# Optimization experiments

Measured on AMD Instinct MI355X. Metric: run time of the kernel, lower is better.

The kernel has to match this reference:

```python
import jax, jax.numpy as jnp
import numpy as np

# ---- static hash-grid config (mirrors init_kwargs) ----
RANGE = 1.0
DIM = 3
N_LEVELS = 16
F_PER_LEVEL = 2
LOG2_HASHMAP = 15
HASHMAP_SIZE = 1 << LOG2_HASHMAP
BASE_RES = 16
FINEST_RES = 512
RANK = 4
PRIMES = np.array([1, 2654435761, 805459861], dtype=np.uint32)


def _resolutions():
    # N_l = floor(base * b^l), b = exp((ln(Nmax)-ln(Nmin))/(L-1))  (Instant-NGP eq. 2-3)
    b = np.exp((np.log(FINEST_RES) - np.log(BASE_RES)) / (N_LEVELS - 1))
    return np.floor(BASE_RES * b ** np.arange(N_LEVELS)).astype(np.float32)


def setup_inputs() -> dict:
    key = jax.random.key(0)
    k1, k2, k3 = jax.random.split(key, 3)
    x = jax.random.uniform(k1, (524288, DIM), dtype=jnp.float32)  # in [-range, range]
    # LoRA factors; small init like hash-grid tables (~1e-2 scale)
    table_A = jax.random.normal(k2, (N_LEVELS, HASHMAP_SIZE, RANK), dtype=jnp.float32) * 1e-2
    table_B = jax.random.normal(k3, (N_LEVELS, RANK, F_PER_LEVEL), dtype=jnp.float32) * 1e-1
    return {"x": x, "table_A": table_A, "table_B": table_B}


def reference(x, table_A, table_B):
    # wrapper: normalize to [0,1]
    xn = (x + RANGE) / (2.0 * RANGE)                         # [N,3]
    res = jnp.asarray(_resolutions())                        # [L]

    # materialize tiny per-level tables from LoRA factors: [L, S, F]
    tables = jnp.einsum('lsr,lrf->lsf', table_A, table_B)

    xl = xn[None, :, :] * res[:, None, None]                 # [L,N,3]
    xf = jnp.floor(xl)
    w = xl - xf                                              # [L,N,3] trilinear weights
    xi = xf.astype(jnp.uint32)                               # [L,N,3]

    # 2^3 corner offsets
    corners = jnp.array([[(c >> d) & 1 for d in range(DIM)] for c in range(2 ** DIM)],
                        dtype=jnp.uint32)                    # [8,3]

    pos = xi[:, :, None, :] + corners[None, None, :, :]      # [L,N,8,3]
    primes = jnp.asarray(PRIMES)
    h = (pos[..., 0] * primes[0]) ^ (pos[..., 1] * primes[1]) ^ (pos[..., 2] * primes[2])
    idx = (h & jnp.uint32(HASHMAP_SIZE - 1)).astype(jnp.int32)  # [L,N,8]

    # per-level gather: [L,N,8,F]
    feats = jax.vmap(lambda t, i: t[i])(tables, idx)

    # trilinear weights per corner: prod over dims of (w or 1-w)
    wc = jnp.prod(jnp.where(corners[None, None, :, :] == 1,
                            w[:, :, None, :], 1.0 - w[:, :, None, :]), axis=-1)  # [L,N,8]

    out_l = jnp.sum(feats * wc[..., None], axis=2)           # [L,N,F]
    out = jnp.transpose(out_l, (1, 0, 2)).reshape(x.shape[0], N_LEVELS * F_PER_LEVEL)
    return out.astype(jnp.float32)
```

## Files before the change

kernel.cpp:

```cpp
#include <hip/hip_runtime.h>
#include <hip/hip_fp16.h>
#include <math.h>
#include <stdint.h>
#include <stddef.h>

#define NLEVELS 16
#define HSIZE   32768
#define LOGH    15
#define RANKK   4
#define PRIME1  2654435761u
#define PRIME2  805459861u

#define BLK2 1024
#define PPB  8192

struct ResArr { float v[NLEVELS]; };

__global__ void build_tables_k(const float* __restrict__ A, const float* __restrict__ B,
                               uint32_t* __restrict__ T) {
    int i = blockIdx.x * blockDim.x + threadIdx.x;
    if (i >= NLEVELS * HSIZE) return;
    int l = i >> LOGH;
    const float4 a = *reinterpret_cast<const float4*>(A + (size_t)i * RANKK);
    const float* b = B + l * (RANKK * 2);
    float f0 = a.x * b[0] + a.y * b[2] + a.z * b[4] + a.w * b[6];
    float f1 = a.x * b[1] + a.y * b[3] + a.z * b[5] + a.w * b[7];
    __half2 h = __floats2half2_rn(f0, f1);
    T[i] = *reinterpret_cast<uint32_t*>(&h);
}

__global__ __launch_bounds__(BLK2)
void encode_level_k(const float* __restrict__ x, const uint32_t* __restrict__ T,
                    float* __restrict__ dst_base, int nPoints, int directOut,
                    ResArr res) {
    __shared__ uint32_t lds[HSIZE];
    const int l     = blockIdx.x & (NLEVELS - 1);
    const int chunk = blockIdx.x >> 4;

    const uint32_t* Tl = T + (size_t)l * HSIZE;
    for (int i = threadIdx.x; i < HSIZE / 4; i += BLK2) {
        reinterpret_cast<uint4*>(lds)[i] = reinterpret_cast<const uint4*>(Tl)[i];
    }
    __syncthreads();

    const float r = res.v[l];
    const int base = chunk * PPB;
    float* dst;
    size_t stride;
    if (directOut) { dst = dst_base + 2 * l;                      stride = 32; }
    else           { dst = dst_base + (size_t)l * nPoints * 2;    stride = 2;  }

    for (int k = 0; k < PPB; k += BLK2) {
        int n = base + k + (int)threadIdx.x;
        if (n >= nPoints) break;
        float xn0 = (x[3 * n + 0] + 1.0f) * 0.5f;
        float xn1 = (x[3 * n + 1] + 1.0f) * 0.5f;
        float xn2 = (x[3 * n + 2] + 1.0f) * 0.5f;
        float xl0 = xn0 * r, xl1 = xn1 * r, xl2 = xn2 * r;
        float fl0 = floorf(xl0), fl1 = floorf(xl1), fl2 = floorf(xl2);
        float w0 = xl0 - fl0, w1 = xl1 - fl1, w2 = xl2 - fl2;
        uint32_t i0 = (uint32_t)fl0, i1 = (uint32_t)fl1, i2 = (uint32_t)fl2;

        uint32_t hx0 = i0,          hx1 = i0 + 1u;
        uint32_t hy0 = i1 * PRIME1, hy1 = hy0 + PRIME1;
        uint32_t hz0 = i2 * PRIME2, hz1 = hz0 + PRIME2;

        float w0a = 1.0f - w0, w1a = 1.0f - w1, w2a = 1.0f - w2;
        float wxy00 = w0a * w1a, wxy10 = w0 * w1a, wxy01 = w0a * w1, wxy11 = w0 * w1;

        float acc0 = 0.0f, acc1 = 0.0f;
#pragma unroll
        for (int c = 0; c < 8; ++c) {
            uint32_t h = ((c & 1) ? hx1 : hx0) ^ ((c & 2) ? hy1 : hy0) ^ ((c & 4) ? hz1 : hz0);
            uint32_t pk = lds[h & (HSIZE - 1)];
            __half2 h2 = *reinterpret_cast<__half2*>(&pk);
            float2 f = __half22float2(h2);
            float wxy = (c & 2) ? ((c & 1) ? wxy11 : wxy01) : ((c & 1) ? wxy10 : wxy00);
            float wc = wxy * ((c & 4) ? w2 : w2a);
            acc0 = fmaf(f.x, wc, acc0);
            acc1 = fmaf(f.y, wc, acc1);
        }
        *reinterpret_cast<float2*>(dst + (size_t)n * stride) = make_float2(acc0, acc1);
    }
}

__global__ void merge_k(const float* __restrict__ outT, float* __restrict__ out, int nPoints) {
    int n = blockIdx.x * blockDim.x + threadIdx.x;
    if (n >= nPoints) return;
    const float2* src = reinterpret_cast<const float2*>(outT);
    float4 o[8];
#pragma unroll
    for (int q = 0; q < 8; ++q) {
        float2 a = src[(size_t)(2 * q)     * nPoints + n];
        float2 b = src[(size_t)(2 * q + 1) * nPoints + n];
        o[q] = make_float4(a.x, a.y, b.x, b.y);
    }
    float4* dstv = reinterpret_cast<float4*>(out + (size_t)n * 32);
#pragma unroll
    for (int q = 0; q < 8; ++q) dstv[q] = o[q];
}

__global__ void encode_fallback_k(const float* __restrict__ x, const float* __restrict__ A,
                                  const float* __restrict__ B, float* __restrict__ out,
                                  int nPoints, ResArr res) {
    int n = blockIdx.x * blockDim.x + threadIdx.x;
    if (n >= nPoints) return;
    float xn0 = (x[3 * n + 0] + 1.0f) * 0.5f;
    float xn1 = (x[3 * n + 1] + 1.0f) * 0.5f;
    float xn2 = (x[3 * n + 2] + 1.0f) * 0.5f;
    for (int l = 0; l < NLEVELS; ++l) {
        float r = res.v[l];
        float xl0 = xn0 * r, xl1 = xn1 * r, xl2 = xn2 * r;
        float fl0 = floorf(xl0), fl1 = floorf(xl1), fl2 = floorf(xl2);
        float w0 = xl0 - fl0, w1 = xl1 - fl1, w2 = xl2 - fl2;
        uint32_t i0 = (uint32_t)fl0, i1 = (uint32_t)fl1, i2 = (uint32_t)fl2;
        uint32_t hx0 = i0,          hx1 = i0 + 1u;
        uint32_t hy0 = i1 * PRIME1, hy1 = hy0 + PRIME1;
        uint32_t hz0 = i2 * PRIME2, hz1 = hz0 + PRIME2;
        float w0a = 1.0f - w0, w1a = 1.0f - w1, w2a = 1.0f - w2;
        float wxy00 = w0a * w1a, wxy10 = w0 * w1a, wxy01 = w0a * w1, wxy11 = w0 * w1;
        const float* b = B + l * 8;
        float b00 = b[0], b01 = b[1], b10 = b[2], b11 = b[3];
        float b20 = b[4], b21 = b[5], b30 = b[6], b31 = b[7];
        float acc0 = 0.0f, acc1 = 0.0f;
#pragma unroll
        for (int c = 0; c < 8; ++c) {
            uint32_t h = ((c & 1) ? hx1 : hx0) ^ ((c & 2) ? hy1 : hy0) ^ ((c & 4) ? hz1 : hz0);
            uint32_t idx = h & (HSIZE - 1);
            float4 a = *reinterpret_cast<const float4*>(A + ((size_t)l * HSIZE + idx) * RANKK);
            float fe0 = a.x * b00 + a.y * b10 + a.z * b20 + a.w * b30;
            float fe1 = a.x * b01 + a.y * b11 + a.z * b21 + a.w * b31;
            float wxy = (c & 2) ? ((c & 1) ? wxy11 : wxy01) : ((c & 1) ? wxy10 : wxy00);
            float wc = wxy * ((c & 4) ? w2 : w2a);
            acc0 = fmaf(fe0, wc, acc0);
            acc1 = fmaf(fe1, wc, acc1);
        }
        out[(size_t)n * 32 + 2 * l + 0] = acc0;
        out[(size_t)n * 32 + 2 * l + 1] = acc1;
    }
}

extern "C" void kernel_launch(void* const* d_in, const int* in_sizes, int n_in,
                              void* d_out, int out_size, void* d_ws, size_t ws_size,
                              hipStream_t stream) {
    const float* x = (const float*)d_in[0];
    const float* A = (const float*)d_in[1];
    const float* B = (const float*)d_in[2];
    float* out = (float*)d_out;
    int nPoints = in_sizes[0] / 3;

    ResArr ra;
    {
        double b = exp((log(512.0) - log(16.0)) / 15.0);
        for (int l = 0; l < NLEVELS; ++l)
            ra.v[l] = (float)floor(16.0 * pow(b, (double)l));
    }

    const size_t tblBytes  = (size_t)NLEVELS * HSIZE * sizeof(uint32_t);
    const size_t outTBytes = (size_t)NLEVELS * (size_t)nPoints * 2 * sizeof(float);

    if (ws_size >= tblBytes) {
        uint32_t* T = (uint32_t*)d_ws;
        int nb1 = (NLEVELS * HSIZE + 255) / 256;
        build_tables_k<<<nb1, 256, 0, stream>>>(A, B, T);
        int chunks = (nPoints + PPB - 1) / PPB;
        if (ws_size >= tblBytes + outTBytes) {
            float* outT = (float*)((char*)d_ws + tblBytes);
            encode_level_k<<<chunks * NLEVELS, BLK2, 0, stream>>>(x, T, outT, nPoints, 0, ra);
            merge_k<<<(nPoints + 255) / 256, 256, 0, stream>>>(outT, out, nPoints);
        } else {
            encode_level_k<<<chunks * NLEVELS, BLK2, 0, stream>>>(x, T, out, nPoints, 1, ra);
        }
    } else {
        encode_fallback_k<<<(nPoints + 255) / 256, 256, 0, stream>>>(x, A, B, out, nPoints, ra);
    }
}
```

Before: 138.6 us.

## Fuse all levels into one kernel per point block with async LDS loads

Replaces the per-level encode kernel and the separate transpose/merge kernel with a single kernel. Each block keeps its points in registers and iterates over all 16 levels, streaming each level's half-precision table into LDS via global_load_lds. Each block then writes the full 32-float output row directly. This removes the intermediate level-major buffer and its extra write/read pass. In exchange, every block reloads all 16 tables, and table loads are serialized with compute behind barriers, with only one block per CU.

```diff
diff --git a/kernel.cpp b/kernel.cpp
--- a/kernel.cpp
+++ b/kernel.cpp
@@ -11,10 +11,14 @@
 #define PRIME1  2654435761u
 #define PRIME2  805459861u
 
-#define BLK2 1024
-#define PPB  8192
+#define BLK  1024
+#define PTS  2
+#define PPB  (BLK * PTS)
 
 struct ResArr { float v[NLEVELS]; };
+
+typedef __attribute__((address_space(1))) const uint32_t gu32;
+typedef __attribute__((address_space(3))) uint32_t lu32;
 
 __global__ void build_tables_k(const float* __restrict__ A, const float* __restrict__ B,
                                uint32_t* __restrict__ T) {
@@ -29,75 +33,86 @@
     T[i] = *reinterpret_cast<uint32_t*>(&h);
 }
 
-__global__ __launch_bounds__(BLK2)
-void encode_level_k(const float* __restrict__ x, const uint32_t* __restrict__ T,
-                    float* __restrict__ dst_base, int nPoints, int directOut,
-                    ResArr res) {
+__global__ __launch_bounds__(BLK)
+void encode_all_k(const float* __restrict__ x, const uint32_t* __restrict__ T,
+                  float* __restrict__ out, int nPoints, ResArr res) {
     __shared__ uint32_t lds[HSIZE];
-    const int l     = blockIdx.x & (NLEVELS - 1);
-    const int chunk = blockIdx.x >> 4;
+    const int t    = threadIdx.x;
+    const int base = blockIdx.x * PPB;
 
-    const uint32_t* Tl = T + (size_t)l * HSIZE;
-    for (int i = threadIdx.x; i < HSIZE / 4; i += BLK2) {
-        reinterpret_cast<uint4*>(lds)[i] = reinterpret_cast<const uint4*>(Tl)[i];
+    int   n[PTS];
+    bool  valid[PTS];
+    float xn0[PTS], xn1[PTS], xn2[PTS];
+#pragma unroll
+    for (int p = 0; p < PTS; ++p) {
+        n[p] = base + p * BLK + t;
+        valid[p] = (n[p] < nPoints);
+        int m = valid[p] ? n[p] : 0;
+        xn0[p] = (x[3 * m + 0] + 1.0f) * 0.5f;
+        xn1[p] = (x[3 * m + 1] + 1.0f) * 0.5f;
+        xn2[p] = (x[3 * m + 2] + 1.0f) * 0.5f;
     }
-    __syncthreads();
 
-    const float r = res.v[l];
-    const int base = chunk * PPB;
-    float* dst;
-    size_t stride;
-    if (directOut) { dst = dst_base + 2 * l;                      stride = 32; }
-    else           { dst = dst_base + (size_t)l * nPoints * 2;    stride = 2;  }
+    float acc[PTS][NLEVELS * 2];
+#pragma unroll
+    for (int p = 0; p < PTS; ++p)
+#pragma unroll
+        for (int q = 0; q < NLEVELS * 2; ++q) acc[p][q] = 0.0f;
 
-    for (int k = 0; k < PPB; k += BLK2) {
-        int n = base + k + (int)threadIdx.x;
-        if (n >= nPoints) break;
-        float xn0 = (x[3 * n + 0] + 1.0f) * 0.5f;
-        float xn1 = (x[3 * n + 1] + 1.0f) * 0.5f;
-        float xn2 = (x[3 * n + 2] + 1.0f) * 0.5f;
-        float xl0 = xn0 * r, xl1 = xn1 * r, xl2 = xn2 * r;
-        float fl0 = floorf(xl0), fl1 = floorf(xl1), fl2 = floorf(xl2);
-        float w0 = xl0 - fl0, w1 = xl1 - fl1, w2 = xl2 - fl2;
-        uint32_t i0 = (uint32_t)fl0, i1 = (uint32_t)fl1, i2 = (uint32_t)fl2;
+#pragma unroll
+    for (int l = 0; l < NLEVELS; ++l) {
+        if (l) __syncthreads();
+        {
+            const uint32_t* Tl = T + (size_t)l * HSIZE;
+#pragma unroll
+            for (int k = 0; k < HSIZE / (BLK * 4); ++k) {
+                int i = (k * BLK + t) * 4;
+                __builtin_amdgcn_global_load_lds((gu32*)(Tl + i), (lu32*)(lds + i), 16, 0, 0);
+            }
+        }
+        __syncthreads();
 
-        uint32_t hx0 = i0,          hx1 = i0 + 1u;
-        uint32_t hy0 = i1 * PRIME1, hy1 = hy0 + PRIME1;
-        uint32_t hz0 = i2 * PRIME2, hz1 = hz0 + PRIME2;
+        const float r = res.v[l];
+#pragma unroll
+        for (int p = 0; p < PTS; ++p) {
+            float xl0 = xn0[p] * r, xl1 = xn1[p] * r, xl2 = xn2[p] * r;
+            float fl0 = floorf(xl0), fl1 = floorf(xl1), fl2 = floorf(xl2);
+            float w0 = xl0 - fl0, w1 = xl1 - fl1, w2 = xl2 - fl2;
+            uint32_t i0 = (uint32_t)fl0, i1 = (uint32_t)fl1, i2 = (uint32_t)fl2;
 
-        float w0a = 1.0f - w0, w1a = 1.0f - w1, w2a = 1.0f - w2;
-        float wxy00 = w0a * w1a, wxy10 = w0 * w1a, wxy01 = w0a * w1, wxy11 = w0 * w1;
+            uint32_t hx0 = i0,          hx1 = i0 + 1u;
+            uint32_t hy0 = i1 * PRIME1, hy1 = hy0 + PRIME1;
+            uint32_t hz0 = i2 * PRIME2, hz1 = hz0 + PRIME2;
 
-        float acc0 = 0.0f, acc1 = 0.0f;
+            float w0a = 1.0f - w0, w1a = 1.0f - w1, w2a = 1.0f - w2;
+            float wxy00 = w0a * w1a, wxy10 = w0 * w1a, wxy01 = w0a * w1, wxy11 = w0 * w1;
+
+            float a0 = 0.0f, a1 = 0.0f;
 #pragma unroll
-        for (int c = 0; c < 8; ++c) {
-            uint32_t h = ((c & 1) ? hx1 : hx0) ^ ((c & 2) ? hy1 : hy0) ^ ((c & 4) ? hz1 : hz0);
-            uint32_t pk = lds[h & (HSIZE - 1)];
-            __half2 h2 = *reinterpret_cast<__half2*>(&pk);
-            float2 f = __half22float2(h2);
-            float wxy = (c & 2) ? ((c & 1) ? wxy11 : wxy01) : ((c & 1) ? wxy10 : wxy00);
-            float wc = wxy * ((c & 4) ? w2 : w2a);
-            acc0 = fmaf(f.x, wc, acc0);
-            acc1 = fmaf(f.y, wc, acc1);
+            for (int c = 0; c < 8; ++c) {
+                uint32_t h = ((c & 1) ? hx1 : hx0) ^ ((c & 2) ? hy1 : hy0) ^ ((c & 4) ? hz1 : hz0);
+                uint32_t pk = lds[h & (HSIZE - 1)];
+                __half2 h2 = *reinterpret_cast<__half2*>(&pk);
+                float2 f = __half22float2(h2);
+                float wxy = (c & 2) ? ((c & 1) ? wxy11 : wxy01) : ((c & 1) ? wxy10 : wxy00);
+                float wc = wxy * ((c & 4) ? w2 : w2a);
+                a0 = fmaf(f.x, wc, a0);
+                a1 = fmaf(f.y, wc, a1);
+            }
+            acc[p][2 * l + 0] = a0;
+            acc[p][2 * l + 1] = a1;
         }
-        *reinterpret_cast<float2*>(dst + (size_t)n * stride) = make_float2(acc0, acc1);
     }
-}
 
-__global__ void merge_k(const float* __restrict__ outT, float* __restrict__ out, int nPoints) {
-    int n = blockIdx.x * blockDim.x + threadIdx.x;
-    if (n >= nPoints) return;
-    const float2* src = reinterpret_cast<const float2*>(outT);
-    float4 o[8];
 #pragma unroll
-    for (int q = 0; q < 8; ++q) {
-        float2 a = src[(size_t)(2 * q)     * nPoints + n];
-        float2 b = src[(size_t)(2 * q + 1) * nPoints + n];
-        o[q] = make_float4(a.x, a.y, b.x, b.y);
+    for (int p = 0; p < PTS; ++p) {
+        if (!valid[p]) continue;
+        float4* dst = reinterpret_cast<float4*>(out + (size_t)n[p] * (NLEVELS * 2));
+#pragma unroll
+        for (int q = 0; q < 8; ++q)
+            dst[q] = make_float4(acc[p][4 * q + 0], acc[p][4 * q + 1],
+                                 acc[p][4 * q + 2], acc[p][4 * q + 3]);
     }
-    float4* dstv = reinterpret_cast<float4*>(out + (size_t)n * 32);
-#pragma unroll
-    for (int q = 0; q < 8; ++q) dstv[q] = o[q];
 }
 
 __global__ void encode_fallback_k(const float* __restrict__ x, const float* __restrict__ A,
@@ -156,21 +171,14 @@
             ra.v[l] = (float)floor(16.0 * pow(b, (double)l));
     }
 
-    const size_t tblBytes  = (size_t)NLEVELS * HSIZE * sizeof(uint32_t);
-    const size_t outTBytes = (size_t)NLEVELS * (size_t)nPoints * 2 * sizeof(float);
+    const size_t tblBytes = (size_t)NLEVELS * HSIZE * sizeof(uint32_t);
 
     if (ws_size >= tblBytes) {
         uint32_t* T = (uint32_t*)d_ws;
         int nb1 = (NLEVELS * HSIZE + 255) / 256;
         build_tables_k<<<nb1, 256, 0, stream>>>(A, B, T);
-        int chunks = (nPoints + PPB - 1) / PPB;
-        if (ws_size >= tblBytes + outTBytes) {
-            float* outT = (float*)((char*)d_ws + tblBytes);
-            encode_level_k<<<chunks * NLEVELS, BLK2, 0, stream>>>(x, T, outT, nPoints, 0, ra);
-            merge_k<<<(nPoints + 255) / 256, 256, 0, stream>>>(outT, out, nPoints);
-        } else {
-            encode_level_k<<<chunks * NLEVELS, BLK2, 0, stream>>>(x, T, out, nPoints, 1, ra);
-        }
+        int blocks = (nPoints + PPB - 1) / PPB;
+        encode_all_k<<<blocks, BLK, 0, stream>>>(x, T, out, nPoints, ra);
     } else {
         encode_fallback_k<<<(nPoints + 255) / 256, 256, 0, stream>>>(x, A, B, out, nPoints, ra);
     }
```

Measured after the change: 365.2 us. 164% more time.
